# Kernel tuning notes

Measured on AMD Instinct MI355X. Metric: run time of the kernel, lower is better.

Reference implementation:

```python
import jax, jax.numpy as jnp
import numpy as np

INPUT_DIM = 1024
GRID_SIZE = 5
SPLINE_ORDER = 3
GRID_MIN, GRID_MAX = -1.5, 1.5
NUM_BASIS = GRID_SIZE + SPLINE_ORDER  # 8
LN_EPS = 1e-5


def _spline_grid():
    # grid = arange(-spline_order, grid_size+spline_order+1)*h + grid_min, per input dim
    h = (GRID_MAX - GRID_MIN) / GRID_SIZE
    g = jnp.arange(-SPLINE_ORDER, GRID_SIZE + SPLINE_ORDER + 1, dtype=jnp.float32) * h + GRID_MIN  # [12]
    return jnp.broadcast_to(g, (INPUT_DIM, g.shape[0]))  # [D, 12]


def _rbf_grid():
    return jnp.linspace(GRID_MIN, GRID_MAX, NUM_BASIS, dtype=jnp.float32)  # [8]


def _b_splines(x):
    # x: [B, D] -> bases [B, D, grid_size+spline_order]
    grid = _spline_grid()  # [D, G]
    xe = x[..., None]  # [B, D, 1]
    bases = ((xe >= grid[:, :-1]) & (xe < grid[:, 1:])).astype(x.dtype)  # [B, D, G-1]
    for k in range(1, SPLINE_ORDER + 1):
        left = (xe - grid[:, :-(k + 1)]) / (grid[:, k:-1] - grid[:, :-(k + 1)])
        right = (grid[:, k + 1:] - xe) / (grid[:, k + 1:] - grid[:, 1:-k])
        bases = left * bases[:, :, :-1] + right * bases[:, :, 1:]
    return bases  # [B, D, NUM_BASIS]


def setup_inputs() -> dict:
    key = jax.random.key(0)
    k1, k2, k3 = jax.random.split(key, 3)
    B, D, O = 8192, INPUT_DIM, 1024
    x = jax.random.normal(k1, (B, D), dtype=jnp.float32)
    ln_weight = jnp.ones((D,), dtype=jnp.float32)
    ln_bias = jnp.zeros((D,), dtype=jnp.float32)
    # kaiming_uniform(a=sqrt(5)) ~ U(-1/sqrt(fan_in), 1/sqrt(fan_in))
    base_weight = jax.random.uniform(k2, (O, D), jnp.float32, -1.0, 1.0) / np.sqrt(D)
    spline_weight = jax.random.uniform(k3, (O, D * NUM_BASIS), jnp.float32, -1.0, 1.0) / np.sqrt(D * NUM_BASIS)
    return {"x": x, "ln_weight": ln_weight, "ln_bias": ln_bias,
            "base_weight": base_weight, "spline_weight": spline_weight}


def reference(x, ln_weight, ln_bias, base_weight, spline_weight):
    B = x.shape[0]
    # LayerNorm
    mu = jnp.mean(x, axis=-1, keepdims=True)
    var = jnp.mean((x - mu) ** 2, axis=-1, keepdims=True)
    xn = (x - mu) * jax.lax.rsqrt(var + LN_EPS) * ln_weight + ln_bias  # [B, D]
    # base branch: SiLU + linear
    base_out = jax.nn.silu(xn) @ base_weight.T  # [B, O]
    # spline branch
    spl = _b_splines(xn).reshape(B, -1)  # [B, D*8]
    spline_out = spl @ spline_weight.T
    # rbf branch (same weight)
    denom = (GRID_MAX - GRID_MIN) / (NUM_BASIS - 1)
    rbf = jnp.exp(-(((xn[..., None] - _rbf_grid()) / denom) ** 2)).reshape(B, -1)  # [B, D*8]
    rbf_out = rbf @ spline_weight.T
    return base_out + rbf_out + spline_out
```

## Files before the change

kernel.cpp:

```cpp
#include <hip/hip_runtime.h>

#define B_ROWS 8192
#define D_IN   1024
#define NOUT   1024
#define KB     1024
#define KS     8192
#define GT     128
#define GK     64
#define GKS    128

#define TBL_N  2048
#define TBL_X0 (-5.5f)
#define TBL_W  11.0f

typedef __attribute__((ext_vector_type(4))) float f32x4;
typedef __attribute__((ext_vector_type(4))) int   i32x4;
typedef __attribute__((ext_vector_type(8))) short bf16x8;

#define SCALE_F 63.5f
#define SCALE_W 11494.728f

__device__ __forceinline__ unsigned short f2bf(float f) {
  union { float f; unsigned u; } v; v.f = f;
  unsigned r = v.u + 0x7fffu + ((v.u >> 16) & 1u);
  return (unsigned short)(r >> 16);
}

__device__ __forceinline__ unsigned pk4(float a, float b, float c, float d, float s) {
  int qa = (int)rintf(fminf(fmaxf(a * s, -127.f), 127.f));
  int qb = (int)rintf(fminf(fmaxf(b * s, -127.f), 127.f));
  int qc = (int)rintf(fminf(fmaxf(c * s, -127.f), 127.f));
  int qd = (int)rintf(fminf(fmaxf(d * s, -127.f), 127.f));
  return (unsigned)(qa & 255) | ((unsigned)(qb & 255) << 8) |
         ((unsigned)(qc & 255) << 16) | ((unsigned)(qd & 255) << 24);
}

__device__ __forceinline__ void load_lds16(const void* g, void* l) {
  __builtin_amdgcn_global_load_lds(
      (const __attribute__((address_space(1))) unsigned int*)g,
      (__attribute__((address_space(3))) unsigned int*)l, 16, 0, 0);
}

__device__ __forceinline__ void barrier_raw() {
  asm volatile("" ::: "memory");
  __builtin_amdgcn_s_barrier();
  asm volatile("" ::: "memory");
}

__global__ __launch_bounds__(256) void tbl_kernel(unsigned char* __restrict__ T) {
  const int k = blockIdx.x * 256 + threadIdx.x;
  const float xn = TBL_X0 + (TBL_W / TBL_N) * k;
  float b[11];
#pragma unroll
  for (int j = 0; j < 11; ++j) {
    const float gj = 0.6f * j - 3.3f;
    b[j] = (xn >= gj && xn < gj + 0.6f) ? 1.f : 0.f;
  }
#pragma unroll
  for (int kk = 1; kk <= 3; ++kk) {
    const float inv = 1.f / (0.6f * kk);
#pragma unroll
    for (int j = 0; j <= 10 - kk; ++j) {
      const float gj = 0.6f * j - 3.3f;
      b[j] = (xn - gj) * inv * b[j] + (gj + 0.6f * (kk + 1) - xn) * inv * b[j + 1];
    }
  }
  float f[8];
#pragma unroll
  for (int j = 0; j < 8; ++j) {
    const float c = -1.5f + (3.f / 7.f) * j;
    const float tt = (xn - c) * (7.f / 3.f);
    f[j] = b[j] + __expf(-tt * tt);
  }
  *reinterpret_cast<uint2*>(T + (size_t)k * 8) =
      make_uint2(pk4(f[0], f[1], f[2], f[3], SCALE_F),
                 pk4(f[4], f[5], f[6], f[7], SCALE_F));
}

__global__ __launch_bounds__(256) void wconv_b(
    const float* __restrict__ bw, unsigned short* __restrict__ Wb) {
  const size_t idx = ((size_t)blockIdx.x * 256 + threadIdx.x) * 4;
  float4 f = *reinterpret_cast<const float4*>(bw + idx);
  union { unsigned short us[4]; uint2 u2; } o;
  o.us[0] = f2bf(f.x); o.us[1] = f2bf(f.y); o.us[2] = f2bf(f.z); o.us[3] = f2bf(f.w);
  *reinterpret_cast<uint2*>(Wb + idx) = o.u2;
}

__global__ __launch_bounds__(256) void wconv_s(
    const float* __restrict__ sw, unsigned char* __restrict__ Ws) {
  const size_t base = ((size_t)blockIdx.x * 256 + threadIdx.x) * 8;
  float4 v0 = *reinterpret_cast<const float4*>(sw + base);
  float4 v1 = *reinterpret_cast<const float4*>(sw + base + 4);
  *reinterpret_cast<uint2*>(Ws + base) =
      make_uint2(pk4(v0.x, v0.y, v0.z, v0.w, SCALE_W),
                 pk4(v1.x, v1.y, v1.z, v1.w, SCALE_W));
}

__global__ __launch_bounds__(256) void feat_kernel(
    const float* __restrict__ x, const float* __restrict__ lnw,
    const float* __restrict__ lnb, const unsigned char* __restrict__ T,
    unsigned short* __restrict__ Fb, unsigned char* __restrict__ Fs, int row0) {
  const int row = row0 + blockIdx.x;
  const float* xr = x + (size_t)row * D_IN;
  const int t = threadIdx.x;
  float v[4];
  float s = 0.f, s2 = 0.f;
#pragma unroll
  for (int i = 0; i < 4; ++i) {
    v[i] = xr[t + 256 * i];
    s += v[i];
    s2 += v[i] * v[i];
  }
#pragma unroll
  for (int off = 32; off > 0; off >>= 1) {
    s += __shfl_xor(s, off);
    s2 += __shfl_xor(s2, off);
  }
  __shared__ float red[8];
  const int wid = t >> 6;
  if ((t & 63) == 0) { red[wid] = s; red[4 + wid] = s2; }
  __syncthreads();
  s  = red[0] + red[1] + red[2] + red[3];
  s2 = red[4] + red[5] + red[6] + red[7];
  const float mu = s * (1.f / D_IN);
  const float var = s2 * (1.f / D_IN) - mu * mu;
  const float rstd = rsqrtf(var + 1e-5f);
  unsigned short* fbr = Fb + (size_t)blockIdx.x * KB;
  unsigned char*  fsr = Fs + (size_t)blockIdx.x * KS;
#pragma unroll
  for (int i = 0; i < 4; ++i) {
    const int d = t + 256 * i;
    const float xn = (v[i] - mu) * rstd * lnw[d] + lnb[d];
    const float e = __expf(-xn);
    fbr[d] = f2bf(xn * __builtin_amdgcn_rcpf(1.f + e));
    int ti = (int)rintf((xn - TBL_X0) * (TBL_N / TBL_W));
    ti = min(max(ti, 0), TBL_N - 1);
    *reinterpret_cast<uint2*>(fsr + d * 8) =
        *reinterpret_cast<const uint2*>(T + (size_t)ti * 8);
  }
}

__global__ __launch_bounds__(256, 2) void gemm_fused(
    const unsigned char* __restrict__ Fs, const unsigned char* __restrict__ Ws,
    const unsigned short* __restrict__ Fb, const unsigned short* __restrict__ Wb,
    float* __restrict__ C, int row0) {
  __shared__ __align__(16) char smem[65536];
  unsigned char* As8 = (unsigned char*)smem;
  unsigned char* Bs8 = (unsigned char*)(smem + 32768);
  const int t = threadIdx.x;
  const int w = t >> 6, l = t & 63;
  const int wr = w >> 1, wc = w & 1;
  const int id = blockIdx.x;
  const int nbm = gridDim.x >> 3;
  int bm, bn;
  if ((nbm & 7) == 0) {
    const int c = id & 7, j = id >> 3, q = nbm >> 3;
    bm = c + 8 * (j % q);
    bn = j / q;
  } else { bm = id % nbm; bn = id / nbm; }

  const int hi = l >> 4, l15 = l & 15, rs = l & 7;

  i32x4 acc[4][4] = {};
  {
    const size_t Ab = (size_t)bm * GT * KS;
    const size_t Bb = (size_t)bn * GT * KS;
    auto stage = [&](int buf, int k0) {
#pragma unroll
      for (int i = 0; i < 4; ++i) {
        const int ch = i * 256 + t;
        const int r = ch >> 3, c = ch & 7;
        load_lds16(Fs + Ab + (size_t)r * KS + k0 + ((c ^ (r & 7)) * 16),
                   As8 + buf * 16384 + ch * 16);
      }
#pragma unroll
      for (int i = 0; i < 4; ++i) {
        const int ch = i * 256 + t;
        const int r = ch >> 3, c = ch & 7;
        load_lds16(Ws + Bb + (size_t)r * KS + k0 + ((c ^ (r & 7)) * 16),
                   Bs8 + buf * 16384 + ch * 16);
      }
    };
    const int c0 = (hi ^ rs) * 16;
    const int c1 = ((4 + hi) ^ rs) * 16;
    i32x4 a0[4], a1[4], b0[4], b1[4];
    auto dsread = [&](int buf) {
      const char* Asb = (const char*)(As8 + buf * 16384);
      const char* Bsb = (const char*)(Bs8 + buf * 16384);
#pragma unroll
      for (int m = 0; m < 4; ++m) {
        a0[m] = *reinterpret_cast<const i32x4*>(Asb + (wr * 64 + l15 + m * 16) * 128 + c0);
        a1[m] = *reinterpret_cast<const i32x4*>(Asb + (wr * 64 + l15 + m * 16) * 128 + c1);
      }
#pragma unroll
      for (int n = 0; n < 4; ++n) {
        b0[n] = *reinterpret_cast<const i32x4*>(Bsb + (wc * 64 + l15 + n * 16) * 128 + c0);
        b1[n] = *reinterpret_cast<const i32x4*>(Bsb + (wc * 64 + l15 + n * 16) * 128 + c1);
      }
    };
    auto domfma = [&]() {
      __builtin_amdgcn_s_setprio(1);
#pragma unroll
      for (int m = 0; m < 4; ++m)
#pragma unroll
        for (int n = 0; n < 4; ++n)
          acc[m][n] = __builtin_amdgcn_mfma_i32_16x16x64_i8(a0[m], b0[n], acc[m][n], 0, 0, 0);
#pragma unroll
      for (int m = 0; m < 4; ++m)
#pragma unroll
        for (int n = 0; n < 4; ++n)
          acc[m][n] = __builtin_amdgcn_mfma_i32_16x16x64_i8(a1[m], b1[n], acc[m][n], 0, 0, 0);
      __builtin_amdgcn_s_setprio(0);
    };
    const int NT = KS / GKS;
    stage(0, 0);
    int cur = 0;
    for (int tt = 0; tt < NT; ++tt) {
      asm volatile("s_waitcnt vmcnt(0)" ::: "memory");
      barrier_raw();
      if (tt + 1 < NT) stage(cur ^ 1, (tt + 1) * GKS);
      dsread(cur);
      __builtin_amdgcn_sched_barrier(0);
      domfma();
      cur ^= 1;
    }
  }
  barrier_raw();

  f32x4 accf[4][4] = {};
  {
    const size_t Abase = (size_t)bm * GT * KB;
    const size_t Bbase = (size_t)bn * GT * KB;
    auto stage = [&](int buf, int k0) {
#pragma unroll
      for (int i = 0; i < 4; ++i) {
        const int ch = i * 256 + t;
        const int r = ch >> 3, c = ch & 7;
        load_lds16(Fb + Abase + (size_t)r * KB + k0 + ((c ^ (r & 7)) * 8),
                   As8 + buf * 16384 + ch * 16);
      }
#pragma unroll
      for (int i = 0; i < 4; ++i) {
        const int ch = i * 256 + t;
        const int r = ch >> 3, c = ch & 7;
        load_lds16(Wb + Bbase + (size_t)r * KB + k0 + ((c ^ (r & 7)) * 8),
                   Bs8 + buf * 16384 + ch * 16);
      }
    };
    bf16x8 a0[4], b0[4], a1[4], b1[4];
    auto dsread = [&](int buf) {
      const char* Asb = (const char*)(As8 + buf * 16384);
      const char* Bsb = (const char*)(Bs8 + buf * 16384);
      const int cb0 = (hi ^ rs) * 16;
      const int cb1 = ((4 + hi) ^ rs) * 16;
#pragma unroll
      for (int m = 0; m < 4; ++m) {
        a0[m] = *reinterpret_cast<const bf16x8*>(Asb + (wr * 64 + l15 + m * 16) * 128 + cb0);
        a1[m] = *reinterpret_cast<const bf16x8*>(Asb + (wr * 64 + l15 + m * 16) * 128 + cb1);
      }
#pragma unroll
      for (int n = 0; n < 4; ++n) {
        b0[n] = *reinterpret_cast<const bf16x8*>(Bsb + (wc * 64 + l15 + n * 16) * 128 + cb0);
        b1[n] = *reinterpret_cast<const bf16x8*>(Bsb + (wc * 64 + l15 + n * 16) * 128 + cb1);
      }
    };
    auto domfma = [&]() {
      __builtin_amdgcn_s_setprio(1);
#pragma unroll
      for (int m = 0; m < 4; ++m)
#pragma unroll
        for (int n = 0; n < 4; ++n)
          accf[m][n] = __builtin_amdgcn_mfma_f32_16x16x32_bf16(a0[m], b0[n], accf[m][n], 0, 0, 0);
#pragma unroll
      for (int m = 0; m < 4; ++m)
#pragma unroll
        for (int n = 0; n < 4; ++n)
          accf[m][n] = __builtin_amdgcn_mfma_f32_16x16x32_bf16(a1[m], b1[n], accf[m][n], 0, 0, 0);
      __builtin_amdgcn_s_setprio(0);
    };
    const int NT = KB / GK;
    stage(0, 0);
    int cur = 0;
    for (int tt = 0; tt < NT; ++tt) {
      asm volatile("s_waitcnt vmcnt(0)" ::: "memory");
      barrier_raw();
      if (tt + 1 < NT) stage(cur ^ 1, (tt + 1) * GK);
      dsread(cur);
      __builtin_amdgcn_sched_barrier(0);
      domfma();
      cur ^= 1;
    }
  }

  const float sc = 1.0f / (SCALE_F * SCALE_W);
  const int crow0 = row0 + bm * GT + wr * 64 + hi * 4;
  const int ccol0 = bn * GT + wc * 64 + l15;
#pragma unroll
  for (int m = 0; m < 4; ++m)
#pragma unroll
    for (int n = 0; n < 4; ++n) {
      float* cp = C + (size_t)(crow0 + m * 16) * NOUT + ccol0 + n * 16;
#pragma unroll
      for (int r = 0; r < 4; ++r)
        cp[(size_t)r * NOUT] = accf[m][n][r] + (float)acc[m][n][r] * sc;
    }
}

extern "C" void kernel_launch(void* const* d_in, const int* in_sizes, int n_in,
                              void* d_out, int out_size, void* d_ws, size_t ws_size,
                              hipStream_t stream) {
  const float* x   = (const float*)d_in[0];
  const float* lnw = (const float*)d_in[1];
  const float* lnb = (const float*)d_in[2];
  const float* bw  = (const float*)d_in[3];
  const float* sw  = (const float*)d_in[4];
  float* out = (float*)d_out;
  char* ws = (char*)d_ws;

  const size_t tbl_bytes = (size_t)TBL_N * 8;
  const size_t wb_bytes = (size_t)NOUT * KB * 2;
  const size_t wsq_bytes = (size_t)NOUT * KS;
  unsigned char*  T   = (unsigned char*)ws;
  unsigned short* Wb  = (unsigned short*)(ws + tbl_bytes);
  unsigned char*  Wsp = (unsigned char*)(ws + tbl_bytes + wb_bytes);
  char* fbase = ws + tbl_bytes + wb_bytes + wsq_bytes;

  const size_t hdr = tbl_bytes + wb_bytes + wsq_bytes;
  const size_t per_row = (size_t)KB * 2 + KS;
  size_t avail = (ws_size > hdr) ? ws_size - hdr : 0;
  long long cm = (long long)(avail / per_row);
  cm &= ~255LL;
  if (cm < 256) cm = 256;
  if (cm > B_ROWS) cm = B_ROWS;
  const int chunkM = (int)cm;
  unsigned short* Fb = (unsigned short*)fbase;
  unsigned char*  Fs = (unsigned char*)(fbase + (size_t)chunkM * KB * 2);

  tbl_kernel<<<TBL_N / 256, 256, 0, stream>>>(T);
  wconv_b<<<(NOUT * KB / 4) / 256, 256, 0, stream>>>(bw, Wb);
  wconv_s<<<(NOUT * KS / 8) / 256, 256, 0, stream>>>(sw, Wsp);
  for (int r0 = 0; r0 < B_ROWS; r0 += chunkM) {
    int rows = B_ROWS - r0; if (rows > chunkM) rows = chunkM;
    feat_kernel<<<rows, 256, 0, stream>>>(x, lnw, lnb, T, Fb, Fs, r0);
    gemm_fused<<<dim3((rows / GT) * (NOUT / GT)), 256, 0, stream>>>(
        Fs, Wsp, Fb, Wb, out, r0);
  }
}
```

Measured before the change: 111.2 us.

## Split GEMM K dimension in two with atomic accumulation and single-buffered LDS

Each output tile is now computed by two blocks, each covering half of the K range for both the int8 spline GEMM and the bf16 base GEMM, with results combined through float atomic adds into an output that is zeroed with a memset first. LDS is cut to a single 32KB buffer, dropping double buffering, and launch bounds rise to four blocks per CU. The aim is more blocks in flight and higher occupancy. In exchange, load/compute overlap inside each block is lost, there is an extra barrier per iteration, and the kernel pays for atomic writes and the memset.

```diff
diff --git a/kernel.cpp b/kernel.cpp
--- a/kernel.cpp
+++ b/kernel.cpp
@@ -140,62 +140,61 @@
   }
 }
 
-__global__ __launch_bounds__(256, 2) void gemm_fused(
+__global__ __launch_bounds__(256, 4) void gemm_fused(
     const unsigned char* __restrict__ Fs, const unsigned char* __restrict__ Ws,
     const unsigned short* __restrict__ Fb, const unsigned short* __restrict__ Wb,
     float* __restrict__ C, int row0) {
-  __shared__ __align__(16) char smem[65536];
+  __shared__ __align__(16) char smem[32768];
   unsigned char* As8 = (unsigned char*)smem;
-  unsigned char* Bs8 = (unsigned char*)(smem + 32768);
+  unsigned char* Bs8 = (unsigned char*)(smem + 16384);
   const int t = threadIdx.x;
   const int w = t >> 6, l = t & 63;
   const int wr = w >> 1, wc = w & 1;
   const int id = blockIdx.x;
-  const int nbm = gridDim.x >> 3;
-  int bm, bn;
-  if ((nbm & 7) == 0) {
-    const int c = id & 7, j = id >> 3, q = nbm >> 3;
-    bm = c + 8 * (j % q);
+  const int nbmk = gridDim.x >> 3;
+  int bmk, bn;
+  if ((nbmk & 7) == 0) {
+    const int c = id & 7, j = id >> 3, q = nbmk >> 3;
+    bmk = c + 8 * (j % q);
     bn = j / q;
-  } else { bm = id % nbm; bn = id / nbm; }
+  } else { bmk = id % nbmk; bn = id / nbmk; }
+  const int bm = bmk >> 1, kp = bmk & 1;
 
   const int hi = l >> 4, l15 = l & 15, rs = l & 7;
 
   i32x4 acc[4][4] = {};
   {
-    const size_t Ab = (size_t)bm * GT * KS;
-    const size_t Bb = (size_t)bn * GT * KS;
-    auto stage = [&](int buf, int k0) {
+    const size_t Ab = (size_t)bm * GT * KS + (size_t)kp * (KS / 2);
+    const size_t Bb = (size_t)bn * GT * KS + (size_t)kp * (KS / 2);
+    auto stage = [&](int k0) {
 #pragma unroll
       for (int i = 0; i < 4; ++i) {
         const int ch = i * 256 + t;
         const int r = ch >> 3, c = ch & 7;
         load_lds16(Fs + Ab + (size_t)r * KS + k0 + ((c ^ (r & 7)) * 16),
-                   As8 + buf * 16384 + ch * 16);
+                   As8 + ch * 16);
       }
 #pragma unroll
       for (int i = 0; i < 4; ++i) {
         const int ch = i * 256 + t;
         const int r = ch >> 3, c = ch & 7;
         load_lds16(Ws + Bb + (size_t)r * KS + k0 + ((c ^ (r & 7)) * 16),
-                   Bs8 + buf * 16384 + ch * 16);
+                   Bs8 + ch * 16);
       }
     };
     const int c0 = (hi ^ rs) * 16;
     const int c1 = ((4 + hi) ^ rs) * 16;
     i32x4 a0[4], a1[4], b0[4], b1[4];
-    auto dsread = [&](int buf) {
-      const char* Asb = (const char*)(As8 + buf * 16384);
-      const char* Bsb = (const char*)(Bs8 + buf * 16384);
+    auto dsread = [&]() {
 #pragma unroll
       for (int m = 0; m < 4; ++m) {
-        a0[m] = *reinterpret_cast<const i32x4*>(Asb + (wr * 64 + l15 + m * 16) * 128 + c0);
-        a1[m] = *reinterpret_cast<const i32x4*>(Asb + (wr * 64 + l15 + m * 16) * 128 + c1);
+        a0[m] = *reinterpret_cast<const i32x4*>(As8 + (wr * 64 + l15 + m * 16) * 128 + c0);
+        a1[m] = *reinterpret_cast<const i32x4*>(As8 + (wr * 64 + l15 + m * 16) * 128 + c1);
       }
 #pragma unroll
       for (int n = 0; n < 4; ++n) {
-        b0[n] = *reinterpret_cast<const i32x4*>(Bsb + (wc * 64 + l15 + n * 16) * 128 + c0);
-        b1[n] = *reinterpret_cast<const i32x4*>(Bsb + (wc * 64 + l15 + n * 16) * 128 + c1);
+        b0[n] = *reinterpret_cast<const i32x4*>(Bs8 + (wc * 64 + l15 + n * 16) * 128 + c0);
+        b1[n] = *reinterpret_cast<const i32x4*>(Bs8 + (wc * 64 + l15 + n * 16) * 128 + c1);
       }
     };
     auto domfma = [&]() {
@@ -212,56 +211,51 @@
           acc[m][n] = __builtin_amdgcn_mfma_i32_16x16x64_i8(a1[m], b1[n], acc[m][n], 0, 0, 0);
       __builtin_amdgcn_s_setprio(0);
     };
-    const int NT = KS / GKS;
-    stage(0, 0);
-    int cur = 0;
+    const int NT = (KS / 2) / GKS;
     for (int tt = 0; tt < NT; ++tt) {
+      stage(tt * GKS);
       asm volatile("s_waitcnt vmcnt(0)" ::: "memory");
       barrier_raw();
-      if (tt + 1 < NT) stage(cur ^ 1, (tt + 1) * GKS);
-      dsread(cur);
+      dsread();
       __builtin_amdgcn_sched_barrier(0);
       domfma();
-      cur ^= 1;
+      barrier_raw();
     }
   }
-  barrier_raw();
 
   f32x4 accf[4][4] = {};
   {
-    const size_t Abase = (size_t)bm * GT * KB;
-    const size_t Bbase = (size_t)bn * GT * KB;
-    auto stage = [&](int buf, int k0) {
+    const size_t Abase = (size_t)bm * GT * KB + (size_t)kp * (KB / 2);
+    const size_t Bbase = (size_t)bn * GT * KB + (size_t)kp * (KB / 2);
+    auto stage = [&](int k0) {
 #pragma unroll
       for (int i = 0; i < 4; ++i) {
         const int ch = i * 256 + t;
         const int r = ch >> 3, c = ch & 7;
         load_lds16(Fb + Abase + (size_t)r * KB + k0 + ((c ^ (r & 7)) * 8),
-                   As8 + buf * 16384 + ch * 16);
+                   As8 + ch * 16);
       }
 #pragma unroll
       for (int i = 0; i < 4; ++i) {
         const int ch = i * 256 + t;
         const int r = ch >> 3, c = ch & 7;
         load_lds16(Wb + Bbase + (size_t)r * KB + k0 + ((c ^ (r & 7)) * 8),
-                   Bs8 + buf * 16384 + ch * 16);
+                   Bs8 + ch * 16);
       }
     };
     bf16x8 a0[4], b0[4], a1[4], b1[4];
-    auto dsread = [&](int buf) {
-      const char* Asb = (const char*)(As8 + buf * 16384);
-      const char* Bsb = (const char*)(Bs8 + buf * 16384);
+    auto dsread = [&]() {
       const int cb0 = (hi ^ rs) * 16;
       const int cb1 = ((4 + hi) ^ rs) * 16;
 #pragma unroll
       for (int m = 0; m < 4; ++m) {
-        a0[m] = *reinterpret_cast<const bf16x8*>(Asb + (wr * 64 + l15 + m * 16) * 128 + cb0);
-        a1[m] = *reinterpret_cast<const bf16x8*>(Asb + (wr * 64 + l15 + m * 16) * 128 + cb1);
+        a0[m] = *reinterpret_cast<const bf16x8*>(As8 + (wr * 64 + l15 + m * 16) * 128 + cb0);
+        a1[m] = *reinterpret_cast<const bf16x8*>(As8 + (wr * 64 + l15 + m * 16) * 128 + cb1);
       }
 #pragma unroll
       for (int n = 0; n < 4; ++n) {
-        b0[n] = *reinterpret_cast<const bf16x8*>(Bsb + (wc * 64 + l15 + n * 16) * 128 + cb0);
-        b1[n] = *reinterpret_cast<const bf16x8*>(Bsb + (wc * 64 + l15 + n * 16) * 128 + cb1);
+        b0[n] = *reinterpret_cast<const bf16x8*>(Bs8 + (wc * 64 + l15 + n * 16) * 128 + cb0);
+        b1[n] = *reinterpret_cast<const bf16x8*>(Bs8 + (wc * 64 + l15 + n * 16) * 128 + cb1);
       }
     };
     auto domfma = [&]() {
@@ -278,17 +272,15 @@
           accf[m][n] = __builtin_amdgcn_mfma_f32_16x16x32_bf16(a1[m], b1[n], accf[m][n], 0, 0, 0);
       __builtin_amdgcn_s_setprio(0);
     };
-    const int NT = KB / GK;
-    stage(0, 0);
-    int cur = 0;
+    const int NT = (KB / 2) / GK;
     for (int tt = 0; tt < NT; ++tt) {
+      stage(tt * GK);
       asm volatile("s_waitcnt vmcnt(0)" ::: "memory");
       barrier_raw();
-      if (tt + 1 < NT) stage(cur ^ 1, (tt + 1) * GK);
-      dsread(cur);
+      dsread();
       __builtin_amdgcn_sched_barrier(0);
       domfma();
-      cur ^= 1;
+      barrier_raw();
     }
   }
 
@@ -302,7 +294,8 @@
       float* cp = C + (size_t)(crow0 + m * 16) * NOUT + ccol0 + n * 16;
 #pragma unroll
       for (int r = 0; r < 4; ++r)
-        cp[(size_t)r * NOUT] = accf[m][n][r] + (float)acc[m][n][r] * sc;
+        unsafeAtomicAdd(&cp[(size_t)r * NOUT],
+                        accf[m][n][r] + (float)acc[m][n][r] * sc);
     }
 }
 
@@ -336,13 +329,14 @@
   unsigned short* Fb = (unsigned short*)fbase;
   unsigned char*  Fs = (unsigned char*)(fbase + (size_t)chunkM * KB * 2);
 
+  hipMemsetAsync(out, 0, (size_t)out_size * sizeof(float), stream);
   tbl_kernel<<<TBL_N / 256, 256, 0, stream>>>(T);
   wconv_b<<<(NOUT * KB / 4) / 256, 256, 0, stream>>>(bw, Wb);
   wconv_s<<<(NOUT * KS / 8) / 256, 256, 0, stream>>>(sw, Wsp);
   for (int r0 = 0; r0 < B_ROWS; r0 += chunkM) {
     int rows = B_ROWS - r0; if (rows > chunkM) rows = chunkM;
     feat_kernel<<<rows, 256, 0, stream>>>(x, lnw, lnb, T, Fb, Fs, r0);
-    gemm_fused<<<dim3((rows / GT) * (NOUT / GT)), 256, 0, stream>>>(
+    gemm_fused<<<dim3((rows / GT) * 2 * (NOUT / GT)), 256, 0, stream>>>(
         Fs, Wsp, Fb, Wb, out, r0);
   }
 }
```

Result: slower. 317.9 us (+186.0%).

## Prepack spline weights into MFMA fragment layout and load B directly to registers

Applied to the files above, without the earlier changes.

The int8 spline weight conversion now writes weights pre-arranged in the per-lane MFMA operand order, so the GEMM loads B fragments straight from global memory into registers instead of staging them through LDS. The A tile moves to a triple-buffered LDS ring, and B registers are double-buffered with partial vmcnt waits so loads overlap compute. This removes the LDS traffic and ds_reads for B. In exchange it uses more registers and depends on global-load latency being hidden, and the hand-counted vmcnt values must match the number of outstanding loads.

```diff
diff --git a/kernel.cpp b/kernel.cpp
--- a/kernel.cpp
+++ b/kernel.cpp
@@ -87,13 +87,26 @@
 }
 
 __global__ __launch_bounds__(256) void wconv_s(
-    const float* __restrict__ sw, unsigned char* __restrict__ Ws) {
-  const size_t base = ((size_t)blockIdx.x * 256 + threadIdx.x) * 8;
-  float4 v0 = *reinterpret_cast<const float4*>(sw + base);
-  float4 v1 = *reinterpret_cast<const float4*>(sw + base + 4);
-  *reinterpret_cast<uint2*>(Ws + base) =
-      make_uint2(pk4(v0.x, v0.y, v0.z, v0.w, SCALE_W),
-                 pk4(v1.x, v1.y, v1.z, v1.w, SCALE_W));
+    const float* __restrict__ sw, unsigned char* __restrict__ Wpk) {
+  const int id = blockIdx.x * 256 + threadIdx.x;
+  const int lane = id & 63;
+  const int row = lane & 15, cw = lane >> 4;
+  const int ks = (id >> 6) & 1;
+  const int tt = (id >> 7) & 63;
+  const int ngrp = id >> 13;
+  const int n = ngrp * 16 + row;
+  const int k = tt * 128 + (ks * 4 + cw) * 16;
+  const float* s = sw + (size_t)n * KS + k;
+  float4 v0 = *reinterpret_cast<const float4*>(s);
+  float4 v1 = *reinterpret_cast<const float4*>(s + 4);
+  float4 v2 = *reinterpret_cast<const float4*>(s + 8);
+  float4 v3 = *reinterpret_cast<const float4*>(s + 12);
+  uint4 o;
+  o.x = pk4(v0.x, v0.y, v0.z, v0.w, SCALE_W);
+  o.y = pk4(v1.x, v1.y, v1.z, v1.w, SCALE_W);
+  o.z = pk4(v2.x, v2.y, v2.z, v2.w, SCALE_W);
+  o.w = pk4(v3.x, v3.y, v3.z, v3.w, SCALE_W);
+  *reinterpret_cast<uint4*>(Wpk + (size_t)id * 16) = o;
 }
 
 __global__ __launch_bounds__(256) void feat_kernel(
@@ -164,67 +177,76 @@
   i32x4 acc[4][4] = {};
   {
     const size_t Ab = (size_t)bm * GT * KS;
-    const size_t Bb = (size_t)bn * GT * KS;
-    auto stage = [&](int buf, int k0) {
+    auto stageA = [&](int slot, int tt) {
+      const int k0 = tt * GKS;
 #pragma unroll
       for (int i = 0; i < 4; ++i) {
         const int ch = i * 256 + t;
         const int r = ch >> 3, c = ch & 7;
         load_lds16(Fs + Ab + (size_t)r * KS + k0 + ((c ^ (r & 7)) * 16),
-                   As8 + buf * 16384 + ch * 16);
-      }
-#pragma unroll
-      for (int i = 0; i < 4; ++i) {
-        const int ch = i * 256 + t;
-        const int r = ch >> 3, c = ch & 7;
-        load_lds16(Ws + Bb + (size_t)r * KS + k0 + ((c ^ (r & 7)) * 16),
-                   Bs8 + buf * 16384 + ch * 16);
+                   As8 + slot * 16384 + ch * 16);
+      }
+    };
+    auto loadB = [&](i32x4* d, int tt) {
+#pragma unroll
+      for (int n = 0; n < 4; ++n) {
+        const unsigned char* p = Ws +
+            (((size_t)(bn * 8 + wc * 4 + n) * 64 + tt) * 2048) + (size_t)l * 16;
+        d[n * 2]     = *reinterpret_cast<const i32x4*>(p);
+        d[n * 2 + 1] = *reinterpret_cast<const i32x4*>(p + 1024);
       }
     };
     const int c0 = (hi ^ rs) * 16;
     const int c1 = ((4 + hi) ^ rs) * 16;
-    i32x4 a0[4], a1[4], b0[4], b1[4];
-    auto dsread = [&](int buf) {
-      const char* Asb = (const char*)(As8 + buf * 16384);
-      const char* Bsb = (const char*)(Bs8 + buf * 16384);
+    i32x4 a0[4], a1[4];
+    auto dsreadA = [&](int slot) {
+      const char* Asb = (const char*)(As8 + slot * 16384);
 #pragma unroll
       for (int m = 0; m < 4; ++m) {
         a0[m] = *reinterpret_cast<const i32x4*>(Asb + (wr * 64 + l15 + m * 16) * 128 + c0);
         a1[m] = *reinterpret_cast<const i32x4*>(Asb + (wr * 64 + l15 + m * 16) * 128 + c1);
       }
-#pragma unroll
-      for (int n = 0; n < 4; ++n) {
-        b0[n] = *reinterpret_cast<const i32x4*>(Bsb + (wc * 64 + l15 + n * 16) * 128 + c0);
-        b1[n] = *reinterpret_cast<const i32x4*>(Bsb + (wc * 64 + l15 + n * 16) * 128 + c1);
-      }
-    };
-    auto domfma = [&]() {
+    };
+    auto domfma = [&](i32x4* b) {
       __builtin_amdgcn_s_setprio(1);
 #pragma unroll
       for (int m = 0; m < 4; ++m)
 #pragma unroll
         for (int n = 0; n < 4; ++n)
-          acc[m][n] = __builtin_amdgcn_mfma_i32_16x16x64_i8(a0[m], b0[n], acc[m][n], 0, 0, 0);
+          acc[m][n] = __builtin_amdgcn_mfma_i32_16x16x64_i8(a0[m], b[n * 2], acc[m][n], 0, 0, 0);
 #pragma unroll
       for (int m = 0; m < 4; ++m)
 #pragma unroll
         for (int n = 0; n < 4; ++n)
-          acc[m][n] = __builtin_amdgcn_mfma_i32_16x16x64_i8(a1[m], b1[n], acc[m][n], 0, 0, 0);
+          acc[m][n] = __builtin_amdgcn_mfma_i32_16x16x64_i8(a1[m], b[n * 2 + 1], acc[m][n], 0, 0, 0);
       __builtin_amdgcn_s_setprio(0);
     };
+    i32x4 bA[8], bB[8];
     const int NT = KS / GKS;
-    stage(0, 0);
-    int cur = 0;
-    for (int tt = 0; tt < NT; ++tt) {
-      asm volatile("s_waitcnt vmcnt(0)" ::: "memory");
-      barrier_raw();
-      if (tt + 1 < NT) stage(cur ^ 1, (tt + 1) * GKS);
-      dsread(cur);
-      __builtin_amdgcn_sched_barrier(0);
-      domfma();
-      cur ^= 1;
-    }
-  }
+    stageA(0, 0);
+    loadB(bA, 0);
+    stageA(1, 1);
+    int slot = 0;
+#define P1_ITER(tt, bthis, bnext)                                            \
+    {                                                                        \
+      if ((tt) + 1 < NT) { asm volatile("s_waitcnt vmcnt(12)" ::: "memory"); } \
+      else               { asm volatile("s_waitcnt vmcnt(8)"  ::: "memory"); } \
+      barrier_raw();                                    \
+      if ((tt) + 1 < NT) loadB(bnext, (tt) + 1);                             \
+      if ((tt) + 2 < NT) { int s2 = slot + 2; if (s2 >= 3) s2 -= 3;          \
+                           stageA(s2, (tt) + 2); }                           \
+      dsreadA(slot);                                                         \
+      __builtin_amdgcn_sched_barrier(0);                                     \
+      domfma(bthis);                                                         \
+      slot = slot + 1; if (slot >= 3) slot = 0;                              \
+    }
+    for (int tt = 0; tt < NT; tt += 2) {
+      P1_ITER(tt, bA, bB);
+      P1_ITER(tt + 1, bB, bA);
+    }
+#undef P1_ITER
+  }
+  asm volatile("s_waitcnt vmcnt(0)" ::: "memory");
   barrier_raw();
 
   f32x4 accf[4][4] = {};
@@ -338,7 +360,7 @@
 
   tbl_kernel<<<TBL_N / 256, 256, 0, stream>>>(T);
   wconv_b<<<(NOUT * KB / 4) / 256, 256, 0, stream>>>(bw, Wb);
-  wconv_s<<<(NOUT * KS / 8) / 256, 256, 0, stream>>>(sw, Wsp);
+  wconv_s<<<(NOUT * KS / 16) / 256, 256, 0, stream>>>(sw, Wsp);
   for (int r0 = 0; r0 < B_ROWS; r0 += chunkM) {
     int rows = B_ROWS - r0; if (rows > chunkM) rows = chunkM;
     feat_kernel<<<rows, 256, 0, stream>>>(x, lnw, lnb, T, Fb, Fs, r0);
```

Measured after the change: 122.0 us. +9.7%, slower.
